# Performance work log

Hardware: AMD Instinct MI355X
Metric: run time of the kernel (lower is better)

The kernel has to match this reference:

```python
import jax, jax.numpy as jnp
import numpy as np

GRID = 64  # 64x64 key grid -> K = 4096


def setup_inputs() -> dict:
    key = jax.random.key(0)
    k1, k2, k3, k4 = jax.random.split(key, 4)
    B, H, Q, K, D = 2, 8, 2048, GRID * GRID, 128
    queries = jax.random.normal(k1, (B, H, Q, D), dtype=jnp.float32)
    keys = jax.random.normal(k2, (B, H, K, D), dtype=jnp.float32)
    # integer (x, y) query positions on the grid
    pos = jax.random.randint(k3, (B, Q, 2), 0, GRID).astype(jnp.int64)
    # relative bias table per head, offsets in [-(GRID-1), GRID-1]
    rel_bias = jax.random.normal(k4, (H, 2 * GRID - 1, 2 * GRID - 1), dtype=jnp.float32)
    # key grid coordinates (row-major flattened 64x64 grid)
    ar = jnp.arange(K)
    grid_x = (ar % GRID).astype(jnp.int64)
    grid_y = (ar // GRID).astype(jnp.int64)
    return {"queries": queries, "keys": keys, "pos": pos, "rel_bias": rel_bias,
            "grid_x": grid_x, "grid_y": grid_y}


def reference(queries, keys, pos, rel_bias, grid_x, grid_y):
    # queries: [B,H,Q,D], keys: [B,H,K,D], pos: [B,Q,2] int,
    # rel_bias: [H,2G-1,2G-1], grid_x/grid_y: [K] int
    D = queries.shape[-1]
    scale = jnp.asarray(1.0 / np.sqrt(D), dtype=queries.dtype)
    scores = jnp.einsum('bhqd,bhkd->bhqk', queries, keys) * scale  # [B,H,Q,K]
    Hb, Wb = rel_bias.shape[-2], rel_bias.shape[-1]
    cy, cx = (Hb - 1) // 2, (Wb - 1) // 2
    # relative offsets, shifted to table indices: [B,Q,K]
    dy = grid_y[None, None, :] - pos[:, :, 1][:, :, None] + cy
    dx = grid_x[None, None, :] - pos[:, :, 0][:, :, None] + cx
    dy = jnp.clip(dy, 0, Hb - 1)
    dx = jnp.clip(dx, 0, Wb - 1)
    flat = (dy * Wb + dx).astype(jnp.int32)  # [B,Q,K]
    # gather per-head bias: [H, B, Q, K] -> [B, H, Q, K]
    bias = jnp.take(rel_bias.reshape(rel_bias.shape[0], -1), flat, axis=1)
    scores = scores + jnp.transpose(bias, (1, 0, 2, 3))
    return jax.nn.softmax(scores, axis=-1)
```

## Files before the change

### kernel.cpp

```cpp
#include <hip/hip_runtime.h>
#include <hip/hip_bf16.h>

typedef __attribute__((ext_vector_type(8))) short short8;
typedef __attribute__((ext_vector_type(4))) float f32x4;

constexpr int Bn = 2, Hn = 8, NQ = 2048, NK = 4096, Dd = 128, Wt = 127;
constexpr int QT = 64, KT = 64;
constexpr int SPLITS = 8, K1_TILES = 8, NC2 = 8;
constexpr int NROWS = Bn * Hn * NQ;
constexpr float SCALE = 0.08838834764831845f;
constexpr float LOG2E = 1.4426950408889634f;
constexpr float S2 = SCALE * LOG2E;
constexpr float BSHIFT = 12.0f * LOG2E;

constexpr size_t WS_SUMS = 0;
constexpr size_t WS_K = 1u << 20;
constexpr size_t WS_Q = WS_K + (size_t)Bn * Hn * NK * Dd * 2;
constexpr size_t WS_B = WS_Q + (size_t)Bn * Hn * NQ * Dd * 2;

constexpr int KELEM = Bn * Hn * NK * Dd;
constexpr int QELEM = Bn * Hn * NQ * Dd;
constexpr int BELEM = Hn * Wt * Wt;
constexpr int KBLK = KELEM / 2048;
constexpr int QBLK = QELEM / 2048;
constexpr int BBLK = (BELEM + 2047) / 2048;

__device__ __forceinline__ short bf16r(float f) {
  union { float f; unsigned u; } v; v.f = f;
  unsigned r = v.u + 0x7fffu + ((v.u >> 16) & 1u);
  return (short)(r >> 16);
}

__device__ __forceinline__ float exp2hw(float x) {
  float r;
  asm("v_exp_f32 %0, %1" : "=v"(r) : "v"(x));
  return r;
}

__global__ __launch_bounds__(256)
void prep_kernel(const float* __restrict__ Km, const float* __restrict__ Qm,
                 const float* __restrict__ Bias, short* __restrict__ wsK,
                 short* __restrict__ wsQ, float* __restrict__ wsB) {
  const int bid = blockIdx.x, tid = threadIdx.x;
  if (bid < KBLK) {
    size_t i = (size_t)bid * 2048 + tid * 8;
    float4 f0 = *(const float4*)(Km + i);
    float4 f1 = *(const float4*)(Km + i + 4);
    short8 v;
    v[0] = bf16r(f0.x); v[1] = bf16r(f0.y); v[2] = bf16r(f0.z); v[3] = bf16r(f0.w);
    v[4] = bf16r(f1.x); v[5] = bf16r(f1.y); v[6] = bf16r(f1.z); v[7] = bf16r(f1.w);
    *(short8*)(wsK + i) = v;
  } else if (bid < KBLK + QBLK) {
    size_t i = (size_t)(bid - KBLK) * 2048 + tid * 8;
    float4 f0 = *(const float4*)(Qm + i);
    float4 f1 = *(const float4*)(Qm + i + 4);
    short8 v;
    v[0] = bf16r(f0.x); v[1] = bf16r(f0.y); v[2] = bf16r(f0.z); v[3] = bf16r(f0.w);
    v[4] = bf16r(f1.x); v[5] = bf16r(f1.y); v[6] = bf16r(f1.z); v[7] = bf16r(f1.w);
    *(short8*)(wsQ + i) = v;
  } else {
    int i = (bid - KBLK - QBLK) * 2048 + tid * 8;
#pragma unroll
    for (int j = 0; j < 8; j++)
      if (i + j < BELEM) wsB[i + j] = Bias[i + j] * LOG2E - BSHIFT;
  }
}

__device__ __forceinline__ void stage_async(int tid, const short* __restrict__ kp,
                                            int kt0, short* buf) {
  const int wave = tid >> 6, lane = tid & 63;
#pragma unroll
  for (int c = 0; c < 4; c++) {
    const int db = c * 4096 + wave * 1024 + lane * 16;
    const int row = db >> 8;
    const int scol = ((db >> 4) & 15) ^ (row & 7);
    const short* src = kp + (size_t)(kt0 + row) * Dd + scol * 8;
    __builtin_amdgcn_global_load_lds(
        (const __attribute__((address_space(1))) void*)src,
        (__attribute__((address_space(3))) void*)(buf + ((c * 4096 + wave * 1024) >> 1)),
        16, 0, 0);
  }
}

__device__ __forceinline__ short8 loadKfrag(const short* buf, int f, int kc,
                                            int l15, int g) {
  const int krow = f * 16 + l15;
  const int byte = (krow << 8) + ((((kc << 2) + g) ^ (krow & 7)) << 4);
  return *(const short8*)((const char*)buf + byte);
}

__global__ __launch_bounds__(256, 4)
void rga_sum_kernel(const short* __restrict__ wsK, const short* __restrict__ wsQ,
                    const int* __restrict__ Pos, const float* __restrict__ wsB,
                    float* __restrict__ sums) {
  __shared__ short lds[2][KT * Dd];
  const int tid = threadIdx.x, wave = tid >> 6, lane = tid & 63;
  const int l15 = lane & 15, g = lane >> 4;
  const int x0 = blockIdx.x;
  const int x = (x0 & 7) * 512 + (x0 >> 3);
  const int qt = x & 31, split = (x >> 5) & 7, bh = x >> 8;
  const int b = bh >> 3, h = bh & 7;

  const short* kp = wsK + (size_t)bh * NK * Dd;
  const short* qp = wsQ + (size_t)bh * NQ * Dd;
  const float* bp = wsB + (size_t)h * Wt * Wt;

  const int q = qt * QT + wave * 16 + l15;
  short8 qfrag[4];
#pragma unroll
  for (int kc = 0; kc < 4; kc++)
    qfrag[kc] = *(const short8*)(qp + (size_t)q * Dd + kc * 32 + g * 8);
  const int pxo = 63 - Pos[((size_t)b * NQ + q) * 2 + 0];
  const int pyo = 63 - Pos[((size_t)b * NQ + q) * 2 + 1];

  const int kt0 = split * (NK / SPLITS);
  stage_async(tid, kp, kt0, lds[0]);
  asm volatile("s_waitcnt vmcnt(0)" ::: "memory");
  __builtin_amdgcn_s_barrier();
  __builtin_amdgcn_sched_barrier(0);

  float ksum = 0.f;
  for (int t = 0; t < K1_TILES; t++) {
    const int kt = kt0 + t * KT;
    if (t + 1 < K1_TILES) stage_async(tid, kp, kt + KT, lds[(t + 1) & 1]);
    __builtin_amdgcn_sched_barrier(0);
    const short* buf = lds[t & 1];
    const float* brow = bp + ((kt >> 6) + pyo) * Wt + pxo;
#pragma unroll
    for (int f = 0; f < 4; f++) {
      f32x4 acc = {0.f, 0.f, 0.f, 0.f};
#pragma unroll
      for (int kc = 0; kc < 4; kc++)
        acc = __builtin_amdgcn_mfma_f32_16x16x32_bf16(loadKfrag(buf, f, kc, l15, g),
                                                      qfrag[kc], acc, 0, 0, 0);
      const int gx0 = f * 16 + g * 4;
#pragma unroll
      for (int j = 0; j < 4; j++)
        ksum += exp2hw(acc[j] * S2 + brow[gx0 + j]);
    }
    __builtin_amdgcn_s_barrier();
    __builtin_amdgcn_sched_barrier(0);
  }
  ksum += __shfl_xor(ksum, 16, 64);
  ksum += __shfl_xor(ksum, 32, 64);
  if (lane < 16) sums[(size_t)split * NROWS + (size_t)bh * NQ + q] = ksum;
}

__global__ __launch_bounds__(256, 4)
void rga_out_kernel(const short* __restrict__ wsK, const short* __restrict__ wsQ,
                    const int* __restrict__ Pos, const float* __restrict__ wsB,
                    const float* __restrict__ sums, float* __restrict__ Out) {
  __shared__ short lds[2][KT * Dd];
  const int tid = threadIdx.x, wave = tid >> 6, lane = tid & 63;
  const int l15 = lane & 15, g = lane >> 4;
  const int x0 = blockIdx.x;
  const int x = (x0 & 7) * 512 + (x0 >> 3);
  const int qt = x & 31, kc8 = (x >> 5) & 7, bh = x >> 8;
  const int b = bh >> 3, h = bh & 7;

  const short* kp = wsK + (size_t)bh * NK * Dd;
  const short* qp = wsQ + (size_t)bh * NQ * Dd;
  const float* bp = wsB + (size_t)h * Wt * Wt;

  const int q = qt * QT + wave * 16 + l15;
  short8 qfrag[4];
#pragma unroll
  for (int kc = 0; kc < 4; kc++)
    qfrag[kc] = *(const short8*)(qp + (size_t)q * Dd + kc * 32 + g * 8);
  const int pxo = 63 - Pos[((size_t)b * NQ + q) * 2 + 0];
  const int pyo = 63 - Pos[((size_t)b * NQ + q) * 2 + 1];

  float lsum = 0.f;
#pragma unroll
  for (int s = 0; s < SPLITS; s++) lsum += sums[(size_t)s * NROWS + (size_t)bh * NQ + q];
  const float rl = 1.0f / lsum;

  float* orow = Out + ((size_t)bh * NQ + q) * NK;
  const int kbase = kc8 * (KT * NC2);
  stage_async(tid, kp, kbase, lds[0]);
  asm volatile("s_waitcnt vmcnt(0)" ::: "memory");
  __builtin_amdgcn_s_barrier();
  __builtin_amdgcn_sched_barrier(0);

  for (int t = 0; t < NC2; t++) {
    const int kt = kbase + t * KT;
    if (t + 1 < NC2) stage_async(tid, kp, kt + KT, lds[(t + 1) & 1]);
    __builtin_amdgcn_sched_barrier(0);
    const short* buf = lds[t & 1];
    const float* brow = bp + ((kt >> 6) + pyo) * Wt + pxo;
#pragma unroll
    for (int f = 0; f < 4; f++) {
      f32x4 acc = {0.f, 0.f, 0.f, 0.f};
#pragma unroll
      for (int kc = 0; kc < 4; kc++)
        acc = __builtin_amdgcn_mfma_f32_16x16x32_bf16(loadKfrag(buf, f, kc, l15, g),
                                                      qfrag[kc], acc, 0, 0, 0);
      const int gx0 = f * 16 + g * 4;
      f32x4 v;
      v[0] = exp2hw(acc[0] * S2 + brow[gx0 + 0]) * rl;
      v[1] = exp2hw(acc[1] * S2 + brow[gx0 + 1]) * rl;
      v[2] = exp2hw(acc[2] * S2 + brow[gx0 + 2]) * rl;
      v[3] = exp2hw(acc[3] * S2 + brow[gx0 + 3]) * rl;
      __builtin_nontemporal_store(v, (f32x4*)(orow + kt + gx0));
    }
    __builtin_amdgcn_s_barrier();
    __builtin_amdgcn_sched_barrier(0);
  }
}

extern "C" void kernel_launch(void* const* d_in, const int* in_sizes, int n_in,
                              void* d_out, int out_size, void* d_ws, size_t ws_size,
                              hipStream_t stream) {
  const float* q = (const float*)d_in[0];
  const float* k = (const float*)d_in[1];
  const int* pos = (const int*)d_in[2];
  const float* bias = (const float*)d_in[3];
  float* out = (float*)d_out;

  char* wsc = (char*)d_ws;
  float* sums = (float*)(wsc + WS_SUMS);
  short* wsK = (short*)(wsc + WS_K);
  short* wsQ = (short*)(wsc + WS_Q);
  float* wsB = (float*)(wsc + WS_B);

  hipLaunchKernelGGL(prep_kernel, dim3(KBLK + QBLK + BBLK), dim3(256), 0, stream,
                     k, q, bias, wsK, wsQ, wsB);
  hipLaunchKernelGGL(rga_sum_kernel, dim3(Bn * Hn * 32 * SPLITS), dim3(256), 0,
                     stream, wsK, wsQ, pos, wsB, sums);
  hipLaunchKernelGGL(rga_out_kernel, dim3(Bn * Hn * 32 * (NK / (KT * NC2))),
                     dim3(256), 0, stream, wsK, wsQ, pos, wsB, sums, out);
}
```

Measured before the change: 228.8 us.

## Prefetch bias rows into registers one tile ahead and raise MFMA priority

```diff
diff --git a/kernel.cpp b/kernel.cpp
--- a/kernel.cpp
+++ b/kernel.cpp
@@ -115,17 +115,33 @@
 
   const int kt0 = split * (NK / SPLITS);
   stage_async(tid, kp, kt0, lds[0]);
+  float breg[4][4];
+  {
+    const float* brow = bp + ((kt0 >> 6) + pyo) * Wt + pxo;
+#pragma unroll
+    for (int f = 0; f < 4; f++)
+#pragma unroll
+      for (int j = 0; j < 4; j++) breg[f][j] = brow[f * 16 + g * 4 + j];
+  }
   asm volatile("s_waitcnt vmcnt(0)" ::: "memory");
   __builtin_amdgcn_s_barrier();
   __builtin_amdgcn_sched_barrier(0);
 
   float ksum = 0.f;
+#pragma unroll
   for (int t = 0; t < K1_TILES; t++) {
-    const int kt = kt0 + t * KT;
-    if (t + 1 < K1_TILES) stage_async(tid, kp, kt + KT, lds[(t + 1) & 1]);
+    float bnext[4][4];
+    if (t + 1 < K1_TILES) {
+      stage_async(tid, kp, kt0 + (t + 1) * KT, lds[(t + 1) & 1]);
+      const float* brow = bp + (((kt0 + (t + 1) * KT) >> 6) + pyo) * Wt + pxo;
+#pragma unroll
+      for (int f = 0; f < 4; f++)
+#pragma unroll
+        for (int j = 0; j < 4; j++) bnext[f][j] = brow[f * 16 + g * 4 + j];
+    }
     __builtin_amdgcn_sched_barrier(0);
     const short* buf = lds[t & 1];
-    const float* brow = bp + ((kt >> 6) + pyo) * Wt + pxo;
+    __builtin_amdgcn_s_setprio(1);
 #pragma unroll
     for (int f = 0; f < 4; f++) {
       f32x4 acc = {0.f, 0.f, 0.f, 0.f};
@@ -133,13 +149,21 @@
       for (int kc = 0; kc < 4; kc++)
         acc = __builtin_amdgcn_mfma_f32_16x16x32_bf16(loadKfrag(buf, f, kc, l15, g),
                                                       qfrag[kc], acc, 0, 0, 0);
-      const int gx0 = f * 16 + g * 4;
 #pragma unroll
       for (int j = 0; j < 4; j++)
-        ksum += exp2hw(acc[j] * S2 + brow[gx0 + j]);
-    }
-    __builtin_amdgcn_s_barrier();
-    __builtin_amdgcn_sched_barrier(0);
+        ksum += exp2hw(acc[j] * S2 + breg[f][j]);
+    }
+    __builtin_amdgcn_s_setprio(0);
+    __builtin_amdgcn_sched_barrier(0);
+    if (t + 1 < K1_TILES) {
+#pragma unroll
+      for (int f = 0; f < 4; f++)
+#pragma unroll
+        for (int j = 0; j < 4; j++) breg[f][j] = bnext[f][j];
+      asm volatile("s_waitcnt vmcnt(16)" ::: "memory");
+      __builtin_amdgcn_s_barrier();
+      __builtin_amdgcn_sched_barrier(0);
+    }
   }
   ksum += __shfl_xor(ksum, 16, 64);
   ksum += __shfl_xor(ksum, 32, 64);
@@ -178,16 +202,33 @@
   float* orow = Out + ((size_t)bh * NQ + q) * NK;
   const int kbase = kc8 * (KT * NC2);
   stage_async(tid, kp, kbase, lds[0]);
+  float breg[4][4];
+  {
+    const float* brow = bp + ((kbase >> 6) + pyo) * Wt + pxo;
+#pragma unroll
+    for (int f = 0; f < 4; f++)
+#pragma unroll
+      for (int j = 0; j < 4; j++) breg[f][j] = brow[f * 16 + g * 4 + j];
+  }
   asm volatile("s_waitcnt vmcnt(0)" ::: "memory");
   __builtin_amdgcn_s_barrier();
   __builtin_amdgcn_sched_barrier(0);
 
+#pragma unroll
   for (int t = 0; t < NC2; t++) {
     const int kt = kbase + t * KT;
-    if (t + 1 < NC2) stage_async(tid, kp, kt + KT, lds[(t + 1) & 1]);
+    float bnext[4][4];
+    if (t + 1 < NC2) {
+      stage_async(tid, kp, kt + KT, lds[(t + 1) & 1]);
+      const float* brow = bp + (((kt + KT) >> 6) + pyo) * Wt + pxo;
+#pragma unroll
+      for (int f = 0; f < 4; f++)
+#pragma unroll
+        for (int j = 0; j < 4; j++) bnext[f][j] = brow[f * 16 + g * 4 + j];
+    }
     __builtin_amdgcn_sched_barrier(0);
     const short* buf = lds[t & 1];
-    const float* brow = bp + ((kt >> 6) + pyo) * Wt + pxo;
+    __builtin_amdgcn_s_setprio(1);
 #pragma unroll
     for (int f = 0; f < 4; f++) {
       f32x4 acc = {0.f, 0.f, 0.f, 0.f};
@@ -197,14 +238,23 @@
                                                       qfrag[kc], acc, 0, 0, 0);
       const int gx0 = f * 16 + g * 4;
       f32x4 v;
-      v[0] = exp2hw(acc[0] * S2 + brow[gx0 + 0]) * rl;
-      v[1] = exp2hw(acc[1] * S2 + brow[gx0 + 1]) * rl;
-      v[2] = exp2hw(acc[2] * S2 + brow[gx0 + 2]) * rl;
-      v[3] = exp2hw(acc[3] * S2 + brow[gx0 + 3]) * rl;
+      v[0] = exp2hw(acc[0] * S2 + breg[f][0]) * rl;
+      v[1] = exp2hw(acc[1] * S2 + breg[f][1]) * rl;
+      v[2] = exp2hw(acc[2] * S2 + breg[f][2]) * rl;
+      v[3] = exp2hw(acc[3] * S2 + breg[f][3]) * rl;
       __builtin_nontemporal_store(v, (f32x4*)(orow + kt + gx0));
     }
-    __builtin_amdgcn_s_barrier();
-    __builtin_amdgcn_sched_barrier(0);
+    __builtin_amdgcn_s_setprio(0);
+    __builtin_amdgcn_sched_barrier(0);
+    if (t + 1 < NC2) {
+#pragma unroll
+      for (int f = 0; f < 4; f++)
+#pragma unroll
+        for (int j = 0; j < 4; j++) breg[f][j] = bnext[f][j];
+      asm volatile("s_waitcnt vmcnt(32)" ::: "memory");
+      __builtin_amdgcn_s_barrier();
+      __builtin_amdgcn_sched_barrier(0);
+    }
   }
 }
 
```

New measurement: 242.0 us. 1.06x slower.
